# Optimization experiments

Measured on AMD Instinct MI355X. Metric: run time of the kernel, lower is better.

Reference implementation:

```python
import jax, jax.numpy as jnp
import numpy as np
import math

C = 512          # channels
K = 3            # conv kernel size
DILATIONS = (1, 3, 5)
RATIO = 2        # up/down sample ratio
FK = 12          # FIR anti-alias kernel size


def kaiser_sinc_filter1d(cutoff, half_width, kernel_size):
    # BigVGAN alias-free kaiser-windowed sinc lowpass filter
    half_size = kernel_size // 2
    delta_f = 4.0 * half_width
    A = 2.285 * (half_size - 1) * math.pi * delta_f + 7.95
    if A > 50.0:
        beta = 0.1102 * (A - 8.7)
    elif A >= 21.0:
        beta = 0.5842 * (A - 21.0) ** 0.4 + 0.07886 * (A - 21.0)
    else:
        beta = 0.0
    window = np.kaiser(kernel_size, beta)
    if kernel_size % 2 == 0:
        time = np.arange(-half_size, half_size) + 0.5
    else:
        time = np.arange(kernel_size) - half_size
    filt = 2.0 * cutoff * window * np.sinc(2.0 * cutoff * time)
    filt = filt / filt.sum()
    return jnp.asarray(filt, dtype=jnp.float32)

# Up/Down both use cutoff=0.5/ratio, half_width=0.6/ratio, kernel=12
AA_FILTER = kaiser_sinc_filter1d(0.5 / RATIO, 0.6 / RATIO, FK)

UP_PAD = FK // RATIO - 1                               # 5 (replicate pad before transpose conv)
UP_PAD_LEFT = UP_PAD * RATIO + (FK - RATIO) // 2       # 15
UP_PAD_RIGHT = UP_PAD * RATIO + (FK - RATIO + 1) // 2  # 15
DN_PAD_LEFT = FK // 2 - 1                              # 5 (even kernel)
DN_PAD_RIGHT = FK // 2                                 # 6


def _depthwise_conv(x, filt, stride=1, lhs_dilation=1, padding=(0, 0)):
    c = x.shape[1]
    w = jnp.broadcast_to(filt.reshape(1, 1, -1), (c, 1, filt.shape[0]))
    return jax.lax.conv_general_dilated(
        x, w, window_strides=(stride,), padding=[padding],
        lhs_dilation=(lhs_dilation,), dimension_numbers=('NCH', 'OIH', 'NCH'),
        feature_group_count=c)


def upsample2x(x):
    # replicate pad, depthwise transposed conv (lhs-dilated conv w/ flipped kernel), crop, scale
    x = jnp.pad(x, ((0, 0), (0, 0), (UP_PAD, UP_PAD)), mode='edge')
    y = RATIO * _depthwise_conv(x, AA_FILTER[::-1], lhs_dilation=RATIO,
                                padding=(FK - 1, FK - 1))
    return y[..., UP_PAD_LEFT:-UP_PAD_RIGHT]


def downsample2x(x):
    x = jnp.pad(x, ((0, 0), (0, 0), (DN_PAD_LEFT, DN_PAD_RIGHT)), mode='edge')
    return _depthwise_conv(x, AA_FILTER, stride=RATIO)


def snake_log(x, alpha, beta):
    # use_log_scale=True: alpha/beta are exponentiated; x + 1/(b+1e-5) * sin(a*x)^2
    a = jnp.exp(alpha)[None, :, None]
    b = jnp.exp(beta)[None, :, None]
    return x + (1.0 / (b + 1e-5)) * jnp.square(jnp.sin(x * a))


def aliasing_activation(x, alpha, beta):
    return downsample2x(snake_log(upsample2x(x), alpha, beta))


def weight_norm_conv1d(x, v, g, bias, dilation):
    # torch weight_norm dim=0: W[o] = g[o] * v[o] / ||v[o]||
    norm = jnp.sqrt(jnp.sum(v * v, axis=(1, 2), keepdims=True))
    w = g[:, None, None] * v / norm
    pad = (K * dilation - dilation) // 2
    y = jax.lax.conv_general_dilated(
        x, w, window_strides=(1,), padding=[(pad, pad)],
        rhs_dilation=(dilation,), dimension_numbers=('NCH', 'OIH', 'NCH'))
    return y + bias[None, :, None]


def setup_inputs() -> dict:
    key = jax.random.key(0)
    ks = jax.random.split(key, 12)
    B, T = 16, 4096
    return {
        'x': jax.random.normal(ks[0], (B, C, T), dtype=jnp.float32),
        'float_masks': jnp.ones((B, 1, T), dtype=jnp.float32),
        'in_snake_alpha': 0.1 * jax.random.normal(ks[1], (3, C), dtype=jnp.float32),
        'in_snake_beta': 0.1 * jax.random.normal(ks[2], (3, C), dtype=jnp.float32),
        'out_snake_alpha': 0.1 * jax.random.normal(ks[3], (3, C), dtype=jnp.float32),
        'out_snake_beta': 0.1 * jax.random.normal(ks[4], (3, C), dtype=jnp.float32),
        'in_conv_v': 0.05 * jax.random.normal(ks[5], (3, C, C, K), dtype=jnp.float32),
        'in_conv_g': 1.0 + 0.01 * jax.random.normal(ks[6], (3, C), dtype=jnp.float32),
        'in_conv_b': 0.01 * jax.random.normal(ks[7], (3, C), dtype=jnp.float32),
        'out_conv_v': 0.05 * jax.random.normal(ks[8], (3, C, C, K), dtype=jnp.float32),
        'out_conv_g': 1.0 + 0.01 * jax.random.normal(ks[9], (3, C), dtype=jnp.float32),
        'out_conv_b': 0.01 * jax.random.normal(ks[10], (3, C), dtype=jnp.float32),
    }


def reference(x, float_masks, in_snake_alpha, in_snake_beta, out_snake_alpha,
              out_snake_beta, in_conv_v, in_conv_g, in_conv_b, out_conv_v,
              out_conv_g, out_conv_b):
    for i, dilation in enumerate(DILATIONS):
        residuals = x
        x = aliasing_activation(x, in_snake_alpha[i], in_snake_beta[i]) * float_masks
        x = weight_norm_conv1d(x, in_conv_v[i], in_conv_g[i], in_conv_b[i], dilation)
        x = aliasing_activation(x, out_snake_alpha[i], out_snake_beta[i]) * float_masks
        x = weight_norm_conv1d(x, out_conv_v[i], out_conv_g[i], out_conv_b[i], 1)
        x = x + residuals
    return x * float_masks
```

## Files before the change

kernel.cpp:

```cpp
#include <hip/hip_runtime.h>
#include <cmath>

#define BN_ 16
#define CN_ 512
#define TN_ 4096
#define TPAD_ 4112
#define PADR_ 8

typedef float f32x4 __attribute__((ext_vector_type(4)));
typedef __bf16 bf16x8 __attribute__((ext_vector_type(8)));
typedef unsigned short u16x8 __attribute__((ext_vector_type(8)));

struct AAFilt { float g0[6]; float g1[6]; float fE[6]; float fO[6]; };

__device__ __forceinline__ unsigned short f2bf(float f) {
  unsigned u = __builtin_bit_cast(unsigned, f);
  u = (u + 0x7fffu + ((u >> 16) & 1u)) >> 16;
  return (unsigned short)u;
}
__device__ __forceinline__ float bf2f(unsigned short h) {
  return __builtin_bit_cast(float, (unsigned)h << 16);
}

__device__ __forceinline__ void gld16(const void* g, void* l) {
  __builtin_amdgcn_global_load_lds((const __attribute__((address_space(1))) void*)g,
                                   (__attribute__((address_space(3))) void*)l,
                                   16, 0, 0);
}

__global__ __launch_bounds__(256) void prep_w(
    const float* __restrict__ vin, const float* __restrict__ gin,
    const float* __restrict__ vout, const float* __restrict__ gout,
    unsigned short* __restrict__ wpack)
{
  const int o = blockIdx.x;
  const int l = blockIdx.y;
  const int i = l >> 1, oc = l & 1;
  const float* v = (oc ? vout : vin) + (size_t)i * CN_ * CN_ * 3 + (size_t)o * CN_ * 3;
  const float g = (oc ? gout : gin)[i * CN_ + o];
  const int tid = threadIdx.x;

  float a = 0.f;
  for (int j = tid; j < 1536; j += 256) { float x = v[j]; a += x * x; }
  #pragma unroll
  for (int off = 32; off > 0; off >>= 1) a += __shfl_down(a, off);
  __shared__ float red[4];
  if ((tid & 63) == 0) red[tid >> 6] = a;
  __syncthreads();
  const float tot = red[0] + red[1] + red[2] + red[3];
  const float scale = g / sqrtf(tot);
  unsigned short* wl = wpack + (size_t)l * 3 * CN_ * CN_;
  for (int j = tid; j < 1536; j += 256) {
    int c = j / 3, k = j - 3 * c;
    wl[((size_t)k * CN_ + o) * CN_ + c] = f2bf(v[j] * scale);
  }
}

__global__ __launch_bounds__(256) void transpose_in(
    const float* __restrict__ src, unsigned short* __restrict__ dst)
{
  __shared__ float tile[32][33];
  const int b = blockIdx.z, c0 = blockIdx.y * 32, t0 = blockIdx.x * 32;
  const int tx = threadIdx.x & 31, ty = threadIdx.x >> 5;
  const float* s = src + ((size_t)b * CN_ + c0) * TN_ + t0;
  #pragma unroll
  for (int j = 0; j < 32; j += 8) tile[ty + j][tx] = s[(size_t)(ty + j) * TN_ + tx];
  __syncthreads();
  unsigned short* d = dst + ((size_t)b * TN_ + t0) * CN_ + c0;
  #pragma unroll
  for (int j = 0; j < 32; j += 8) d[(size_t)(ty + j) * CN_ + tx] = f2bf(tile[tx][ty + j]);
}

__global__ __launch_bounds__(512) void act_kernel(
    const unsigned short* __restrict__ src, unsigned short* __restrict__ dst,
    const float* __restrict__ alpha, const float* __restrict__ beta,
    const float* __restrict__ mask, AAFilt F)
{
  const int c = threadIdx.x;
  const int b = blockIdx.y;
  const int seg = blockIdx.x;
  const int t0 = seg << 7;
  const float av = expf(alpha[c]);
  const float ib = 1.0f / (expf(beta[c]) + 1e-5f);
  const unsigned short* row = src + (size_t)b * TN_ * CN_ + c;
  unsigned short* drow = dst + (size_t)b * TPAD_ * CN_ + c;
  const float* mrow = mask + (size_t)b * TN_;

  if (seg == 0)  { for (int p = 0; p < PADR_; ++p) drow[(size_t)p * CN_] = 0; }
  if (seg == 31) { for (int p = 0; p < PADR_; ++p) drow[(size_t)(TPAD_ - PADR_ + p) * CN_] = 0; }

  auto ldx = [&](int t) -> float {
    t = t < 0 ? 0 : (t > TN_ - 1 ? TN_ - 1 : t);
    return bf2f(row[(size_t)t * CN_]);
  };

  float xw[6];
  #pragma unroll
  for (int j = 0; j < 6; ++j) xw[j] = ldx(t0 - 5 + j);
  float sE[6], sO[6];
  #pragma unroll
  for (int j = 0; j < 6; ++j) { sE[j] = 0.f; sO[j] = 0.f; }
  float s_last = 0.f;

  auto step = [&](int tau, bool emit) {
    float uO = 0.f, uE = 0.f;
    #pragma unroll
    for (int j = 0; j < 6; ++j) { uO += F.g1[j] * xw[j]; uE += F.g0[j] * xw[j]; }
    float so = __sinf(uO * av); float sOn = uO + ib * so * so;
    float se = __sinf(uE * av); float sEn = uE + ib * se * se;
    if (tau + 2 == TN_ - 1) s_last = sOn;
    if (tau + 2 >= TN_) sOn = s_last;
    if (tau + 3 >= TN_) sEn = s_last;
    #pragma unroll
    for (int j = 0; j < 5; ++j) { sE[j] = sE[j + 1]; sO[j] = sO[j + 1]; }
    sE[5] = sEn; sO[5] = sOn;
    if (emit) {
      float d = 0.f;
      #pragma unroll
      for (int j = 0; j < 6; ++j) d += F.fE[j] * sE[j] + F.fO[j] * sO[j];
      d *= mrow[tau];
      drow[(size_t)(PADR_ + tau) * CN_] = f2bf(d);
    }
    #pragma unroll
    for (int j = 0; j < 5; ++j) xw[j] = xw[j + 1];
    xw[5] = ldx(tau + 6);
  };

  for (int w = 0; w < 5; ++w) step(t0 - 5 + w, false);
  if (t0 == 0) {
    float s0 = sE[3];
    sE[1] = s0; sE[2] = s0;
    sO[1] = s0; sO[2] = s0; sO[3] = s0;
  }
  for (int t = t0; t < t0 + 128; ++t) step(t, true);
}

#define ASZ (144 * 32)
#define BSLOT (128 * 32)

#define VMCNT(n) asm volatile("s_waitcnt vmcnt(" #n ")" ::: "memory")
#define BAR __builtin_amdgcn_s_barrier()
#define PRIO1 __builtin_amdgcn_s_setprio(1)
#define PRIO0 __builtin_amdgcn_s_setprio(0)

#define READ_A4(k) do { \
    _Pragma("unroll") \
    for (int mi_ = 0; mi_ < 4; ++mi_) { \
      const int r_ = rbase[k] + mi_ * 16; \
      const int q_ = q4 ^ ((r_ >> 1) & 3); \
      af[mi_] = __builtin_bit_cast(bf16x8, \
          *(const u16x8*)(A + ((size_t)r_ * 4 + q_) * 8)); \
    } \
  } while (0)

#define READ_B4(slot) do { \
    const unsigned short* Bs_ = lB + (size_t)(slot) * BSLOT; \
    _Pragma("unroll") \
    for (int ni_ = 0; ni_ < 4; ++ni_) { \
      const int ob_ = wn * 64 + ni_ * 16 + l15; \
      const int q_ = q4 ^ ((ob_ >> 1) & 3); \
      bfr[ni_] = __builtin_bit_cast(bf16x8, \
          *(const u16x8*)(Bs_ + ((size_t)ob_ * 4 + q_) * 8)); \
    } \
  } while (0)

#define MFMA16 do { \
    _Pragma("unroll") \
    for (int mi_ = 0; mi_ < 4; ++mi_) { \
      _Pragma("unroll") \
      for (int ni_ = 0; ni_ < 4; ++ni_) \
        acc[mi_][ni_] = __builtin_amdgcn_mfma_f32_16x16x32_bf16( \
            af[mi_], bfr[ni_], acc[mi_][ni_], 0, 0, 0); \
    } \
  } while (0)

template <int MODE, int DIL>
__global__ __launch_bounds__(256, 3) void conv_kernel(
    const unsigned short* __restrict__ act,
    const unsigned short* __restrict__ wp,
    const float* __restrict__ bias,
    const unsigned short* __restrict__ res,
    const float* __restrict__ mask,
    void* __restrict__ outp)
{
  __shared__ __align__(16) unsigned short lA[2 * ASZ];
  __shared__ __align__(16) unsigned short lB[4 * BSLOT];

  const int tid = threadIdx.x;
  const int bid = blockIdx.x;
  const int xcd = bid & 7, j = bid >> 3;
  const int ob = j & 3, tile = j >> 2;
  const int tt = tile * 8 + xcd;
  const int b = tt >> 5;
  const int t0 = (tt & 31) << 7;
  const int o0 = ob << 7;

  const int lane = tid & 63;
  const int wave = tid >> 6;
  const int wm = wave >> 1, wn = wave & 1;
  const int l15 = lane & 15, q4 = lane >> 4;

  const f32x4 zero = {0.f, 0.f, 0.f, 0.f};
  f32x4 acc[4][4];
  #pragma unroll
  for (int a = 0; a < 4; ++a)
    #pragma unroll
    for (int n = 0; n < 4; ++n) acc[a][n] = zero;

  const unsigned short* aBase = act + ((size_t)b * TPAD_ + t0) * CN_;

  int rbase[3];
  #pragma unroll
  for (int k = 0; k < 3; ++k) rbase[k] = wm * 64 + l15 + PADR_ + (k - 1) * DIL;

  auto stageA = [&](unsigned short* Ad, int c0) {
    { int p = tid;       int r = p >> 2, pq = p & 3, gq = pq ^ ((r >> 1) & 3);
      gld16(aBase + (size_t)r * CN_ + c0 + gq * 8, Ad + (size_t)p * 8); }
    { int p = tid + 256; int r = p >> 2, pq = p & 3, gq = pq ^ ((r >> 1) & 3);
      gld16(aBase + (size_t)r * CN_ + c0 + gq * 8, Ad + (size_t)p * 8); }
    if (tid < 64) {
      int p = tid + 512;
      int r = p >> 2, pq = p & 3, gq = pq ^ ((r >> 1) & 3);
      gld16(aBase + (size_t)r * CN_ + c0 + gq * 8, Ad + (size_t)p * 8); }
  };
  auto stageB = [&](int slot, int c0, int k) {
    unsigned short* Bd = lB + (size_t)slot * BSLOT;
    { int p = tid;       int ol = p >> 2, pq = p & 3, gq = pq ^ ((ol >> 1) & 3);
      gld16(wp + ((size_t)(k * CN_) + o0 + ol) * CN_ + c0 + gq * 8,
            Bd + (size_t)p * 8); }
    { int p = tid + 256; int ol = p >> 2, pq = p & 3, gq = pq ^ ((ol >> 1) & 3);
      gld16(wp + ((size_t)(k * CN_) + o0 + ol) * CN_ + c0 + gq * 8,
            Bd + (size_t)p * 8); }
  };

  stageA(lA, 0);
  stageB(0, 0, 0); stageB(1, 0, 1); stageB(2, 0, 2);
  VMCNT(4);
  BAR;

  for (int cb = 0; cb < 15; ++cb) {
    const unsigned short* A = lA + (size_t)(cb & 1) * ASZ;
    unsigned short* An = lA + (size_t)((cb & 1) ^ 1) * ASZ;
    const int c0n = (cb + 1) * 32;
    const int tau = 3 * cb;
    bf16x8 af[4], bfr[4];
    READ_A4(0); READ_B4(tau & 3);
    stageA(An, c0n); stageB((tau + 3) & 3, c0n, 0);
    BAR; PRIO1; MFMA16; PRIO0; VMCNT(6); BAR;
    READ_A4(1); READ_B4((tau + 1) & 3);
    stageB((tau + 4) & 3, c0n, 1);
    BAR; PRIO1; MFMA16; PRIO0; VMCNT(6); BAR;
    READ_A4(2); READ_B4((tau + 2) & 3);
    stageB((tau + 5) & 3, c0n, 2);
    BAR; PRIO1; MFMA16; PRIO0; VMCNT(4); BAR;
  }
  {
    const unsigned short* A = lA + ASZ;
    const int tau = 45;
    bf16x8 af[4], bfr[4];
    READ_A4(0); READ_B4(tau & 3);
    BAR; PRIO1; MFMA16; PRIO0; VMCNT(2); BAR;
    READ_A4(1); READ_B4((tau + 1) & 3);
    BAR; PRIO1; MFMA16; PRIO0; VMCNT(0); BAR;
    READ_A4(2); READ_B4((tau + 2) & 3);
    BAR; PRIO1; MFMA16; PRIO0;
  }

  const int obase = o0 + wn * 64 + l15;
  const int tbase = t0 + wm * 64 + q4 * 4;

  if (MODE == 0) {
    unsigned short* O = (unsigned short*)outp + (size_t)b * TN_ * CN_;
    #pragma unroll
    for (int ni = 0; ni < 4; ++ni) {
      float bv = bias[obase + ni * 16];
      #pragma unroll
      for (int mi = 0; mi < 4; ++mi) {
        #pragma unroll
        for (int r = 0; r < 4; ++r) {
          int t = tbase + mi * 16 + r;
          O[(size_t)t * CN_ + obase + ni * 16] = f2bf(acc[mi][ni][r] + bv);
        }
      }
    }
  } else if (MODE == 1) {
    unsigned short* O = (unsigned short*)outp + (size_t)b * TN_ * CN_;
    const unsigned short* R = res + (size_t)b * TN_ * CN_;
    #pragma unroll
    for (int ni = 0; ni < 4; ++ni) {
      float bv = bias[obase + ni * 16];
      #pragma unroll
      for (int mi = 0; mi < 4; ++mi) {
        #pragma unroll
        for (int r = 0; r < 4; ++r) {
          int t = tbase + mi * 16 + r;
          size_t ix = (size_t)t * CN_ + obase + ni * 16;
          O[ix] = f2bf(acc[mi][ni][r] + bv + bf2f(R[ix]));
        }
      }
    }
  } else {
    float* O = (float*)outp + (size_t)b * CN_ * TN_;
    const unsigned short* R = res + (size_t)b * TN_ * CN_;
    const float* M = mask + (size_t)b * TN_;
    float bv[4];
    #pragma unroll
    for (int ni = 0; ni < 4; ++ni) bv[ni] = bias[obase + ni * 16];
    #pragma unroll
    for (int mi = 0; mi < 4; ++mi) {
      int t = tbase + mi * 16;
      f32x4 mv = *reinterpret_cast<const f32x4*>(M + t);
      #pragma unroll
      for (int ni = 0; ni < 4; ++ni) {
        f32x4 v;
        #pragma unroll
        for (int r = 0; r < 4; ++r)
          v[r] = (acc[mi][ni][r] + bv[ni] + bf2f(R[(size_t)(t + r) * CN_ + obase + ni * 16])) * mv[r];
        *reinterpret_cast<f32x4*>(O + (size_t)(obase + ni * 16) * TN_ + t) = v;
      }
    }
  }
}

static double bi0(double x) {
  double s = 1.0, t = 1.0, q = x * x * 0.25;
  for (int k = 1; k < 50; ++k) { t *= q / ((double)k * (double)k); s += t; if (t < 1e-18 * s) break; }
  return s;
}
static void make_filt(AAFilt* F) {
  const double PI = 3.14159265358979323846;
  double A = 2.285 * 5.0 * PI * 1.2 + 7.95;
  double beta;
  if (A > 50.0) beta = 0.1102 * (A - 8.7);
  else if (A >= 21.0) beta = 0.5842 * pow(A - 21.0, 0.4) + 0.07886 * (A - 21.0);
  else beta = 0.0;
  double i0b = bi0(beta);
  double f[12], sum = 0.0;
  for (int n = 0; n < 12; ++n) {
    double xx = 2.0 * n / 11.0 - 1.0;
    double w = bi0(beta * sqrt(fmax(0.0, 1.0 - xx * xx))) / i0b;
    double tt = (double)(n - 6) + 0.5;
    double arg = 0.5 * tt;
    double snc = sin(PI * arg) / (PI * arg);
    f[n] = 0.5 * w * snc;
    sum += f[n];
  }
  for (int n = 0; n < 12; ++n) f[n] /= sum;
  for (int j = 0; j < 6; ++j) {
    F->g0[j] = (float)(2.0 * f[11 - 2 * j]);
    F->g1[j] = (float)(2.0 * f[10 - 2 * j]);
    F->fE[j] = (float)f[2 * j + 1];
    F->fO[j] = (float)f[2 * j];
  }
}

extern "C" void kernel_launch(void* const* d_in, const int* in_sizes, int n_in,
                              void* d_out, int out_size, void* d_ws, size_t ws_size,
                              hipStream_t stream)
{
  (void)in_sizes; (void)n_in; (void)out_size; (void)ws_size;
  const float* x    = (const float*)d_in[0];
  const float* mask = (const float*)d_in[1];
  const float* inA  = (const float*)d_in[2];
  const float* inB  = (const float*)d_in[3];
  const float* outA = (const float*)d_in[4];
  const float* outB = (const float*)d_in[5];
  const float* vin  = (const float*)d_in[6];
  const float* gin  = (const float*)d_in[7];
  const float* bin  = (const float*)d_in[8];
  const float* vout = (const float*)d_in[9];
  const float* gout = (const float*)d_in[10];
  const float* bout = (const float*)d_in[11];

  char* ws = (char*)d_ws;
  unsigned short* xta  = (unsigned short*)ws;
  unsigned short* xtb  = (unsigned short*)(ws + 67108864);
  unsigned short* actb = (unsigned short*)(ws + 134217728);
  unsigned short* y1   = (unsigned short*)(ws + 134217728 + 67371008);
  unsigned short* wpk  = (unsigned short*)(ws + 134217728 + 67371008 + 67108864);

  AAFilt F; make_filt(&F);

  prep_w<<<dim3(512, 6), dim3(256), 0, stream>>>(vin, gin, vout, gout, wpk);
  transpose_in<<<dim3(128, 16, 16), dim3(256), 0, stream>>>(x, xta);

  act_kernel<<<dim3(32, 16), dim3(512), 0, stream>>>(
      xta, actb, inA + 0 * CN_, inB + 0 * CN_, mask, F);
  conv_kernel<0, 1><<<dim3(2048), dim3(256), 0, stream>>>(
      actb, wpk + (size_t)0 * 3 * CN_ * CN_, bin + 0 * CN_, nullptr, mask, (void*)y1);
  act_kernel<<<dim3(32, 16), dim3(512), 0, stream>>>(
      y1, actb, outA + 0 * CN_, outB + 0 * CN_, mask, F);
  conv_kernel<1, 1><<<dim3(2048), dim3(256), 0, stream>>>(
      actb, wpk + (size_t)1 * 3 * CN_ * CN_, bout + 0 * CN_, xta, mask, (void*)xtb);

  act_kernel<<<dim3(32, 16), dim3(512), 0, stream>>>(
      xtb, actb, inA + 1 * CN_, inB + 1 * CN_, mask, F);
  conv_kernel<0, 3><<<dim3(2048), dim3(256), 0, stream>>>(
      actb, wpk + (size_t)2 * 3 * CN_ * CN_, bin + 1 * CN_, nullptr, mask, (void*)y1);
  act_kernel<<<dim3(32, 16), dim3(512), 0, stream>>>(
      y1, actb, outA + 1 * CN_, outB + 1 * CN_, mask, F);
  conv_kernel<1, 1><<<dim3(2048), dim3(256), 0, stream>>>(
      actb, wpk + (size_t)3 * 3 * CN_ * CN_, bout + 1 * CN_, xtb, mask, (void*)xta);

  act_kernel<<<dim3(32, 16), dim3(512), 0, stream>>>(
      xta, actb, inA + 2 * CN_, inB + 2 * CN_, mask, F);
  conv_kernel<0, 5><<<dim3(2048), dim3(256), 0, stream>>>(
      actb, wpk + (size_t)4 * 3 * CN_ * CN_, bin + 2 * CN_, nullptr, mask, (void*)y1);
  act_kernel<<<dim3(32, 16), dim3(512), 0, stream>>>(
      y1, actb, outA + 2 * CN_, outB + 2 * CN_, mask, F);
  conv_kernel<2, 1><<<dim3(2048), dim3(256), 0, stream>>>(
      actb, wpk + (size_t)5 * 3 * CN_ * CN_, bout + 2 * CN_, xta, mask, d_out);
}
```

Before: 1.095 ms.

## Shrink conv LDS footprint via halo rows in registers and triple-buffered weights

The A tile in LDS drops from 144 to 128 rows. The halo rows that fall outside the tile for the k=0 and k=2 taps are now loaded directly from global memory into a register (eCur/eNxt) and swapped into the MFMA operands. The weight ring buffer shrinks from 4 slots to 3, with the stage and vmcnt schedule reworked to match, and the launch bounds rise from 3 to 4 blocks per CU. The aim is higher occupancy from less LDS per block. The cost is extra per-lane global loads, a tighter prefetch window for weights, and register pressure at the higher occupancy target.

```diff
diff --git a/kernel.cpp b/kernel.cpp
--- a/kernel.cpp
+++ b/kernel.cpp
@@ -1,5 +1,6 @@
 #include <hip/hip_runtime.h>
 #include <cmath>
+#include <cstddef>
 
 #define BN_ 16
 #define CN_ 512
@@ -135,7 +136,7 @@
   for (int t = t0; t < t0 + 128; ++t) step(t, true);
 }
 
-#define ASZ (144 * 32)
+#define ASZ (128 * 32)
 #define BSLOT (128 * 32)
 
 #define VMCNT(n) asm volatile("s_waitcnt vmcnt(" #n ")" ::: "memory")
@@ -146,6 +147,8 @@
 #define READ_A4(k) do { \
     _Pragma("unroll") \
     for (int mi_ = 0; mi_ < 4; ++mi_) { \
+      if ((k) == 0 && mi_ == 0 && wm == 0) { af[0] = eCur; continue; } \
+      if ((k) == 2 && mi_ == 3 && wm == 1) { af[3] = eCur; continue; } \
       const int r_ = rbase[k] + mi_ * 16; \
       const int q_ = q4 ^ ((r_ >> 1) & 3); \
       af[mi_] = __builtin_bit_cast(bf16x8, \
@@ -175,7 +178,7 @@
   } while (0)
 
 template <int MODE, int DIL>
-__global__ __launch_bounds__(256, 3) void conv_kernel(
+__global__ __launch_bounds__(256, 4) void conv_kernel(
     const unsigned short* __restrict__ act,
     const unsigned short* __restrict__ wp,
     const float* __restrict__ bias,
@@ -184,7 +187,7 @@
     void* __restrict__ outp)
 {
   __shared__ __align__(16) unsigned short lA[2 * ASZ];
-  __shared__ __align__(16) unsigned short lB[4 * BSLOT];
+  __shared__ __align__(16) unsigned short lB[3 * BSLOT];
 
   const int tid = threadIdx.x;
   const int bid = blockIdx.x;
@@ -207,21 +210,20 @@
     #pragma unroll
     for (int n = 0; n < 4; ++n) acc[a][n] = zero;
 
-  const unsigned short* aBase = act + ((size_t)b * TPAD_ + t0) * CN_;
+  const unsigned short* aBase8 = act + ((size_t)b * TPAD_ + t0 + PADR_) * CN_;
 
   int rbase[3];
   #pragma unroll
-  for (int k = 0; k < 3; ++k) rbase[k] = wm * 64 + l15 + PADR_ + (k - 1) * DIL;
+  for (int k = 0; k < 3; ++k) rbase[k] = wm * 64 + l15 + (k - 1) * DIL;
+
+  const int erow = wm ? (112 + l15 + DIL) : (l15 - DIL);
+  const unsigned short* eSrc = aBase8 + (ptrdiff_t)erow * CN_ + q4 * 8;
 
   auto stageA = [&](unsigned short* Ad, int c0) {
     { int p = tid;       int r = p >> 2, pq = p & 3, gq = pq ^ ((r >> 1) & 3);
-      gld16(aBase + (size_t)r * CN_ + c0 + gq * 8, Ad + (size_t)p * 8); }
+      gld16(aBase8 + (size_t)r * CN_ + c0 + gq * 8, Ad + (size_t)p * 8); }
     { int p = tid + 256; int r = p >> 2, pq = p & 3, gq = pq ^ ((r >> 1) & 3);
-      gld16(aBase + (size_t)r * CN_ + c0 + gq * 8, Ad + (size_t)p * 8); }
-    if (tid < 64) {
-      int p = tid + 512;
-      int r = p >> 2, pq = p & 3, gq = pq ^ ((r >> 1) & 3);
-      gld16(aBase + (size_t)r * CN_ + c0 + gq * 8, Ad + (size_t)p * 8); }
+      gld16(aBase8 + (size_t)r * CN_ + c0 + gq * 8, Ad + (size_t)p * 8); }
   };
   auto stageB = [&](int slot, int c0, int k) {
     unsigned short* Bd = lB + (size_t)slot * BSLOT;
@@ -233,36 +235,40 @@
             Bd + (size_t)p * 8); }
   };
 
+  bf16x8 eCur = __builtin_bit_cast(bf16x8, *(const u16x8*)(eSrc));
   stageA(lA, 0);
-  stageB(0, 0, 0); stageB(1, 0, 1); stageB(2, 0, 2);
-  VMCNT(4);
+  stageB(0, 0, 0); stageB(1, 0, 1);
+  VMCNT(2);
   BAR;
 
   for (int cb = 0; cb < 15; ++cb) {
     const unsigned short* A = lA + (size_t)(cb & 1) * ASZ;
     unsigned short* An = lA + (size_t)((cb & 1) ^ 1) * ASZ;
-    const int c0n = (cb + 1) * 32;
-    const int tau = 3 * cb;
+    const int c0 = cb * 32, c0n = c0 + 32;
     bf16x8 af[4], bfr[4];
-    READ_A4(0); READ_B4(tau & 3);
-    stageA(An, c0n); stageB((tau + 3) & 3, c0n, 0);
-    BAR; PRIO1; MFMA16; PRIO0; VMCNT(6); BAR;
-    READ_A4(1); READ_B4((tau + 1) & 3);
-    stageB((tau + 4) & 3, c0n, 1);
-    BAR; PRIO1; MFMA16; PRIO0; VMCNT(6); BAR;
-    READ_A4(2); READ_B4((tau + 2) & 3);
-    stageB((tau + 5) & 3, c0n, 2);
-    BAR; PRIO1; MFMA16; PRIO0; VMCNT(4); BAR;
+    bf16x8 eNxt;
+    READ_A4(0); READ_B4(0);
+    stageA(An, c0n); stageB(2, c0, 2);
+    eNxt = __builtin_bit_cast(bf16x8, *(const u16x8*)(eSrc + c0n));
+    BAR; PRIO1; MFMA16; PRIO0; VMCNT(5); BAR;
+    READ_A4(1); READ_B4(1);
+    stageB(0, c0n, 0);
+    BAR; PRIO1; MFMA16; PRIO0; VMCNT(2); BAR;
+    READ_A4(2); READ_B4(2);
+    stageB(1, c0n, 1);
+    BAR; PRIO1; MFMA16; PRIO0; VMCNT(2); BAR;
+    eCur = eNxt;
   }
   {
     const unsigned short* A = lA + ASZ;
-    const int tau = 45;
+    const int c0 = 480;
     bf16x8 af[4], bfr[4];
-    READ_A4(0); READ_B4(tau & 3);
+    READ_A4(0); READ_B4(0);
+    stageB(2, c0, 2);
     BAR; PRIO1; MFMA16; PRIO0; VMCNT(2); BAR;
-    READ_A4(1); READ_B4((tau + 1) & 3);
+    READ_A4(1); READ_B4(1);
     BAR; PRIO1; MFMA16; PRIO0; VMCNT(0); BAR;
-    READ_A4(2); READ_B4((tau + 2) & 3);
+    READ_A4(2); READ_B4(2);
     BAR; PRIO1; MFMA16; PRIO0;
   }
 
```

After: 2.068 ms. +88.9%, slower.
